# Kernel tuning notes

Measured on AMD Instinct MI355X. Metric: run time of the kernel, lower is better.

The kernel has to match this reference:

```python
import jax, jax.numpy as jnp
import numpy as np

NEG_INF = -1e30

def mask_logits(target, mask):
    return target * mask + (1.0 - mask) * NEG_INF

def setup_inputs() -> dict:
    key = jax.random.key(0)
    k1, k2, k3 = jax.random.split(key, 3)
    B, D, Lc, Lq = 32, 256, 2048, 256
    C = jax.random.normal(k1, (B, D, Lc), dtype=jnp.float32)
    Q = jax.random.normal(k2, (B, D, Lq), dtype=jnp.float32)
    cmask = jnp.ones((B, Lc), dtype=jnp.float32)
    qmask = jnp.ones((B, Lq), dtype=jnp.float32)
    lim = np.sqrt(1.0 / D)
    w = jax.random.uniform(k3, (3 * D,), dtype=jnp.float32, minval=-lim, maxval=lim)
    return {"C": C, "Q": Q, "cmask": cmask, "qmask": qmask, "w": w}

def reference(C, Q, cmask, qmask, w):
    # C: (B, D, Lc), Q: (B, D, Lq) -> transpose to (B, L, D)
    Ct = jnp.swapaxes(C, 1, 2)            # (B, Lc, D)
    Qt = jnp.swapaxes(Q, 1, 2)            # (B, Lq, D)
    D = Ct.shape[-1]
    w1, w2, w3 = w[:D], w[D:2 * D], w[2 * D:]
    # S[b,c,q] = Ct[b,c]@w1 + Qt[b,q]@w2 + (Ct[b,c]*w3)@Qt[b,q]
    # (identical to matmul(cat([Ct,Qt,Ct*Qt],-1), w) without the 4-D tensor)
    S = (Ct @ w1)[:, :, None] + (Qt @ w2)[:, None, :] \
        + jnp.einsum('bcd,bqd->bcq', Ct * w3, Qt)     # (B, Lc, Lq)
    qm = qmask[:, None, :]                 # (B, 1, Lq)
    cm = cmask[:, :, None]                 # (B, Lc, 1)
    S1 = jax.nn.softmax(mask_logits(S, qm), axis=2)   # over query dim
    S2 = jax.nn.softmax(mask_logits(S, cm), axis=1)   # over context dim
    A = jnp.einsum('bcq,bqd->bcd', S1, Qt)            # (B, Lc, D)
    Bv = jnp.einsum('bck,bkd->bcd',
                    jnp.einsum('bcq,bkq->bck', S1, S2), Ct)  # (B, Lc, D)
    out = jnp.concatenate([Ct, A, Ct * A, Ct * Bv], axis=2)  # (B, Lc, 4D)
    # dropout omitted (eval mode)
    return jnp.swapaxes(out, 1, 2)         # (B, 4D, Lc)
```

## Files before the change

### kernel.cpp

```cpp
#include <hip/hip_runtime.h>


#define B_ 32
#define D_ 256
#define LC 2048
#define LQ 256
#define KSPLIT 4
#define NEG_INF (-1e30f)

using bf16   = __bf16;
using bf16x4 = __attribute__((ext_vector_type(4))) __bf16;
using bf16x8 = __attribute__((ext_vector_type(8))) __bf16;
using f32x4  = __attribute__((ext_vector_type(4))) float;

static __device__ __forceinline__ f32x4 mfma16(bf16x8 a, bf16x8 b, f32x4 c) {
  return __builtin_amdgcn_mfma_f32_16x16x32_bf16(a, b, c, 0, 0, 0);
}

__global__ __launch_bounds__(256) void qprep(const float* __restrict__ Q,
                                             const float* __restrict__ w,
                                             bf16* __restrict__ Qtb,
                                             bf16* __restrict__ Qb16,
                                             float* __restrict__ bqp) {
  __shared__ float t[64][65];
  __shared__ float pb[4][64];
  const int b  = blockIdx.y;
  const int qt = (blockIdx.x >> 2) * 64;
  const int dtI = blockIdx.x & 3, dt = dtI * 64;
  const int c  = threadIdx.x & 63, r0 = threadIdx.x >> 6;
  const float* Qb = Q + (size_t)b * D_ * LQ;
  bf16* Qcb = Qb16 + (size_t)b * D_ * LQ;
  float partial = 0.f;
#pragma unroll
  for (int r = r0; r < 64; r += 4) {
    const float v = Qb[(size_t)(dt + r) * LQ + qt + c];
    t[r][c] = v;
    Qcb[(size_t)(dt + r) * LQ + qt + c] = (bf16)v;
    partial += v * w[D_ + dt + r];
  }
  pb[r0][c] = partial;
  __syncthreads();
  bf16* O = Qtb + (size_t)b * LQ * D_;
#pragma unroll
  for (int r = r0; r < 64; r += 4)
    O[(size_t)(qt + r) * D_ + dt + c] = (bf16)t[c][r];
  if (r0 == 0)
    bqp[((size_t)(b * 4 + dtI)) * LQ + qt + c] = pb[0][c] + pb[1][c] + pb[2][c] + pb[3][c];
}

__global__ __launch_bounds__(256) void k1_sgemm(
    const float* __restrict__ C, const bf16* __restrict__ Qtb,
    const float* __restrict__ w, const float* __restrict__ cmask,
    const float* __restrict__ qmask, const float* __restrict__ bqp,
    bf16* __restrict__ S1, bf16* __restrict__ S1t,
    float* __restrict__ cpmax, float* __restrict__ cpsum) {
  __shared__ __align__(16) bf16 As[64][72];
  __shared__ __align__(16) bf16 Bs[256][72];
  __shared__ float ared[4][64];
  __shared__ float wred[4][64];
  __shared__ float wsum[4][64];
  __shared__ float cml[64];
  __shared__ float qml[256];
  __shared__ float bql[256];

  const int b = blockIdx.y, ct = blockIdx.x, c0 = ct * 64;
  const int tid = threadIdx.x, lane = tid & 63, wv = tid >> 6;
  const float* Cb = C + (size_t)b * D_ * LC;
  const bf16* Qt = Qtb + (size_t)b * LQ * D_;
  const float* w1 = w;
  const float* w3 = w + 2 * D_;

  if (tid < 64) cml[tid] = cmask[b * LC + c0 + tid];
  qml[tid] = qmask[b * LQ + tid];
  bql[tid] = bqp[(size_t)(b * 4 + 0) * LQ + tid] + bqp[(size_t)(b * 4 + 1) * LQ + tid] +
             bqp[(size_t)(b * 4 + 2) * LQ + tid] + bqp[(size_t)(b * 4 + 3) * LQ + tid];

  f32x4 acc[4][4];
#pragma unroll
  for (int i = 0; i < 4; i++)
#pragma unroll
    for (int j = 0; j < 4; j++) acc[i][j] = {0.f, 0.f, 0.f, 0.f};
  float acc_a = 0.f;

  const int sm = tid & 63;
  const int skg = tid >> 6;

  for (int k0 = 0; k0 < D_; k0 += 64) {
#pragma unroll
    for (int i = 0; i < 16; ++i) {
      const int k = skg * 16 + i, kg = k0 + k;
      const float v = Cb[(size_t)kg * LC + c0 + sm];
      As[sm][k] = (bf16)(v * w3[kg]);
      acc_a += v * w1[kg];
    }
#pragma unroll
    for (int p = 0; p < 8; ++p) {
      const int idx = (p * 256 + tid) * 8;
      const int q = idx >> 6, kk = idx & 63;
      *(bf16x8*)(&Bs[q][kk]) = *(const bf16x8*)(Qt + (size_t)q * D_ + k0 + kk);
    }
    __syncthreads();
#pragma unroll
    for (int kk = 0; kk < 64; kk += 32) {
      bf16x8 af[4], bfr[4];
#pragma unroll
      for (int mi = 0; mi < 4; mi++)
        af[mi] = *(const bf16x8*)(&As[mi * 16 + (lane & 15)][kk + (lane >> 4) * 8]);
#pragma unroll
      for (int ni = 0; ni < 4; ni++)
        bfr[ni] = *(const bf16x8*)(&Bs[wv * 64 + ni * 16 + (lane & 15)][kk + (lane >> 4) * 8]);
#pragma unroll
      for (int mi = 0; mi < 4; mi++)
#pragma unroll
        for (int ni = 0; ni < 4; ni++)
          acc[mi][ni] = mfma16(af[mi], bfr[ni], acc[mi][ni]);
    }
    __syncthreads();
  }

  ared[skg][sm] = acc_a;
  __syncthreads();

  const int r4 = (lane >> 4) * 4;
  const int cn = lane & 15;

#pragma unroll
  for (int mi = 0; mi < 4; mi++)
#pragma unroll
    for (int j = 0; j < 4; j++) {
      const int m = mi * 16 + r4 + j;
      const float aval = ared[0][m] + ared[1][m] + ared[2][m] + ared[3][m];
#pragma unroll
      for (int ni = 0; ni < 4; ni++) {
        const int n = wv * 64 + ni * 16 + cn;
        const bf16 sb = (bf16)(acc[mi][ni][j] + aval + bql[n]);
        acc[mi][ni][j] = (float)sb;
      }
    }

#pragma unroll
  for (int ni = 0; ni < 4; ni++) {
    const int n = wv * 64 + ni * 16 + cn;
    float mx = -3.0e38f;
#pragma unroll
    for (int mi = 0; mi < 4; mi++)
#pragma unroll
      for (int j = 0; j < 4; j++) {
        const int m = mi * 16 + r4 + j;
        const float cmv = cml[m];
        const float lg = acc[mi][ni][j] * cmv + (1.f - cmv) * NEG_INF;
        mx = fmaxf(mx, lg);
      }
    mx = fmaxf(mx, __shfl_xor(mx, 16));
    mx = fmaxf(mx, __shfl_xor(mx, 32));
    float ps = 0.f;
#pragma unroll
    for (int mi = 0; mi < 4; mi++)
#pragma unroll
      for (int j = 0; j < 4; j++) {
        const int m = mi * 16 + r4 + j;
        const float cmv = cml[m];
        const float lg = acc[mi][ni][j] * cmv + (1.f - cmv) * NEG_INF;
        ps += __expf(lg - mx);
      }
    ps += __shfl_xor(ps, 16);
    ps += __shfl_xor(ps, 32);
    if ((lane >> 4) == 0) {
      cpmax[((size_t)(b * 32 + ct)) * LQ + n] = mx;
      cpsum[((size_t)(b * 32 + ct)) * LQ + n] = ps;
    }
  }

#pragma unroll
  for (int mi = 0; mi < 4; mi++)
#pragma unroll
    for (int j = 0; j < 4; j++) {
      float mx = -3.0e38f;
#pragma unroll
      for (int ni = 0; ni < 4; ni++) {
        const int n = wv * 64 + ni * 16 + cn;
        const float qm = qml[n];
        const float lg = acc[mi][ni][j] * qm + (1.f - qm) * NEG_INF;
        mx = fmaxf(mx, lg);
      }
      for (int s = 1; s < 16; s <<= 1) mx = fmaxf(mx, __shfl_xor(mx, s));
      if (cn == 0) wred[wv][mi * 16 + r4 + j] = mx;
    }
  __syncthreads();

  float rmv[4][4];
#pragma unroll
  for (int mi = 0; mi < 4; mi++)
#pragma unroll
    for (int j = 0; j < 4; j++) {
      const int m = mi * 16 + r4 + j;
      const float rm = fmaxf(fmaxf(wred[0][m], wred[1][m]), fmaxf(wred[2][m], wred[3][m]));
      rmv[mi][j] = rm;
      float ps = 0.f;
#pragma unroll
      for (int ni = 0; ni < 4; ni++) {
        const int n = wv * 64 + ni * 16 + cn;
        const float qm = qml[n];
        const float lg = acc[mi][ni][j] * qm + (1.f - qm) * NEG_INF;
        const float e = __expf(lg - rm);
        acc[mi][ni][j] = e;
        ps += e;
      }
      for (int s = 1; s < 16; s <<= 1) ps += __shfl_xor(ps, s);
      if (cn == 0) wsum[wv][m] = ps;
    }
  __syncthreads();

  bf16* S1b = S1 + ((size_t)b * LC + c0) * LQ;
#pragma unroll
  for (int mi = 0; mi < 4; mi++)
#pragma unroll
    for (int j = 0; j < 4; j++) {
      const int m = mi * 16 + r4 + j;
      const float rs = wsum[0][m] + wsum[1][m] + wsum[2][m] + wsum[3][m];
      const float rsl = 1.0f / rs;
      const float f = cml[m] * __expf(rmv[mi][j]);
#pragma unroll
      for (int ni = 0; ni < 4; ni++) {
        const int n = wv * 64 + ni * 16 + cn;
        const float e = acc[mi][ni][j];
        S1b[(size_t)m * LQ + n] = (bf16)(e * rsl);
        Bs[n][m] = (bf16)(e * f);
      }
    }
  __syncthreads();
  bf16* dst = S1t + ((size_t)b * LQ + tid) * LC + c0;
#pragma unroll
  for (int jj = 0; jj < 8; ++jj)
    *(bf16x8*)(dst + jj * 8) = *(const bf16x8*)(&Bs[tid][jj * 8]);
}

__global__ __launch_bounds__(256) void k2_colstats(const float* __restrict__ cpmax,
                                                   const float* __restrict__ cpsum,
                                                   float* __restrict__ cscl) {
  const int b = blockIdx.x, q = threadIdx.x;
  float m = -3.0e38f;
  for (int t = 0; t < 32; t++) m = fmaxf(m, cpmax[(size_t)(b * 32 + t) * LQ + q]);
  float s = 0.f;
  for (int t = 0; t < 32; t++)
    s += cpsum[(size_t)(b * 32 + t) * LQ + q] * __expf(cpmax[(size_t)(b * 32 + t) * LQ + q] - m);
  cscl[b * LQ + q] = __expf(-m) / s;
}

__global__ __launch_bounds__(256, 3) void k3_ugemm(
    const bf16* __restrict__ S1t, const float* __restrict__ C,
    float* __restrict__ Up) {
  const int g = blockIdx.x;
  const int x = g & 7, s = g >> 3;
  const int quad = (s >> 2) * 8 + x;
  const int inner = s & 3;
  const int b = quad >> 2, ks = quad & 3;
  const int qt = inner >> 1, dtI = inner & 1;
  const int mt = qt * 128, nt = dtI * 128;
  const int cbase = ks * (LC / KSPLIT);

  const int tid = threadIdx.x, lane = tid & 63, wv = tid >> 6;
  const int wm = (wv >> 1) * 64, wn = (wv & 1) * 64;
  const int fr = lane & 15, kg = lane >> 4;

  const bf16* Sb = S1t + (size_t)b * LQ * LC;
  const float* Cb = C + (size_t)b * D_ * LC;

  int qrow[4];
#pragma unroll
  for (int mi = 0; mi < 4; mi++) qrow[mi] = mt + wm + mi * 16 + fr;

  f32x4 acc[4][4];
#pragma unroll
  for (int i = 0; i < 4; i++)
#pragma unroll
    for (int j = 0; j < 4; j++) acc[i][j] = {0.f, 0.f, 0.f, 0.f};

#pragma unroll 2
  for (int k0 = 0; k0 < LC / KSPLIT; k0 += 64) {
    const int c8 = cbase + k0 + kg * 8;
    bf16x8 af[4][2];
#pragma unroll
    for (int mi = 0; mi < 4; mi++)
#pragma unroll
      for (int s2 = 0; s2 < 2; ++s2)
        af[mi][s2] = *(const bf16x8*)(Sb + (size_t)qrow[mi] * LC + c8 + s2 * 32);
    bf16x8 bfr[4][2];
#pragma unroll
    for (int ni = 0; ni < 4; ni++) {
      const float* cp = Cb + (size_t)(nt + wn + ni * 16 + fr) * LC + c8;
#pragma unroll
      for (int s2 = 0; s2 < 2; ++s2) {
        const f32x4 v0 = *(const f32x4*)(cp + s2 * 32);
        const f32x4 v1 = *(const f32x4*)(cp + s2 * 32 + 4);
        bf16x8 tt;
#pragma unroll
        for (int e = 0; e < 4; ++e) { tt[e] = (bf16)v0[e]; tt[e + 4] = (bf16)v1[e]; }
        bfr[ni][s2] = tt;
      }
    }
#pragma unroll
    for (int s2 = 0; s2 < 2; ++s2)
#pragma unroll
      for (int mi = 0; mi < 4; mi++)
#pragma unroll
        for (int ni = 0; ni < 4; ni++)
          acc[mi][ni] = mfma16(af[mi][s2], bfr[ni][s2], acc[mi][ni]);
  }

  float* Ub = Up + ((size_t)(ks * B_ + b)) * D_ * LQ;
#pragma unroll
  for (int mi = 0; mi < 4; mi++)
#pragma unroll
    for (int ni = 0; ni < 4; ni++) {
      const int q = mt + wm + mi * 16 + kg * 4;
      const int d = nt + wn + ni * 16 + fr;
      *(f32x4*)(Ub + (size_t)d * LQ + q) = acc[mi][ni];
    }
}

__global__ __launch_bounds__(256) void k3r_reduce(const float* __restrict__ Up,
                                                  const float* __restrict__ cscl,
                                                  bf16* __restrict__ Utb) {
  const size_t NP = (size_t)B_ * D_ * LQ;
  const size_t i4 = ((size_t)blockIdx.x * 256 + threadIdx.x) * 4;
  const int b = (int)(i4 >> 16);
  const int q = (int)(i4 & (LQ - 1));
  f32x4 s = *(const f32x4*)(Up + i4);
#pragma unroll
  for (int p = 1; p < KSPLIT; ++p) {
    const f32x4 v = *(const f32x4*)(Up + p * NP + i4);
    s[0] += v[0]; s[1] += v[1]; s[2] += v[2]; s[3] += v[3];
  }
  const f32x4 sc = *(const f32x4*)(cscl + b * LQ + q);
  bf16x4 o = {(bf16)(s[0] * sc[0]), (bf16)(s[1] * sc[1]),
              (bf16)(s[2] * sc[2]), (bf16)(s[3] * sc[3])};
  *(bf16x4*)(Utb + i4) = o;
}

__global__ __launch_bounds__(256, 3) void k4_final(
    const bf16* __restrict__ S1, const float* __restrict__ C,
    const bf16* __restrict__ Qb16, const bf16* __restrict__ Utb,
    float* __restrict__ out) {
  __shared__ float bounce[64][131];

  const int g = blockIdx.x;
  const int x = g & 7, s = g >> 3;
  const int t = s >> 1, ntI = s & 1;
  const int pair = t * 8 + x;
  const int b = pair >> 5, ct = pair & 31;
  const int c0 = ct * 64, nt = ntI * 128;

  const int tid = threadIdx.x, lane = tid & 63, wv = tid >> 6;
  const int wm = (wv >> 1) * 32, wn = (wv & 1) * 64;
  const int fr = lane & 15, kg = lane >> 4;

  const bf16* S1b = S1 + ((size_t)b * LC + c0) * LQ;
  const float* Cb = C + (size_t)b * D_ * LC;
  const bf16* Qcb = Qb16 + (size_t)b * D_ * LQ;
  const bf16* Ub = Utb + (size_t)b * D_ * LQ;

  f32x4 acc1[2][4], acc2[2][4];
#pragma unroll
  for (int i = 0; i < 2; i++)
#pragma unroll
    for (int j = 0; j < 4; j++) {
      acc1[i][j] = {0.f, 0.f, 0.f, 0.f};
      acc2[i][j] = {0.f, 0.f, 0.f, 0.f};
    }

#pragma unroll
  for (int k = 0; k < 8; ++k) {
    const int q8 = k * 32 + kg * 8;
    const bf16x8 af0 = *(const bf16x8*)(S1b + (size_t)(wm + fr) * LQ + q8);
    const bf16x8 af1 = *(const bf16x8*)(S1b + (size_t)(wm + 16 + fr) * LQ + q8);
#pragma unroll
    for (int ni = 0; ni < 4; ++ni) {
      const int d = nt + wn + ni * 16 + fr;
      const bf16x8 b1 = *(const bf16x8*)(Qcb + (size_t)d * LQ + q8);
      const bf16x8 b2 = *(const bf16x8*)(Ub + (size_t)d * LQ + q8);
      acc1[0][ni] = mfma16(af0, b1, acc1[0][ni]);
      acc1[1][ni] = mfma16(af1, b1, acc1[1][ni]);
      acc2[0][ni] = mfma16(af0, b2, acc2[0][ni]);
      acc2[1][ni] = mfma16(af1, b2, acc2[1][ni]);
    }
  }

  const int r4 = kg * 4;
#pragma unroll
  for (int mi = 0; mi < 2; mi++)
#pragma unroll
    for (int ni = 0; ni < 4; ni++)
#pragma unroll
      for (int j = 0; j < 4; j++)
        bounce[wm + mi * 16 + r4 + j][wn + ni * 16 + fr] = acc1[mi][ni][j];
  __syncthreads();

  const int cq = (tid & 15) * 4;
  const int drb = tid >> 4;
  const size_t outB = (size_t)b * (4 * D_) * LC;
  f32x4 creg[8];
#pragma unroll
  for (int m = 0; m < 8; ++m) {
    const int dr = drb + m * 16;
    const int d = nt + dr;
    f32x4 av;
#pragma unroll
    for (int e = 0; e < 4; ++e) av[e] = bounce[cq + e][dr];
    const f32x4 cv = *(const f32x4*)(Cb + (size_t)d * LC + c0 + cq);
    creg[m] = cv;
    f32x4 ca;
#pragma unroll
    for (int e = 0; e < 4; ++e) ca[e] = cv[e] * av[e];
    *(f32x4*)(out + outB + (size_t)d * LC + c0 + cq) = cv;
    *(f32x4*)(out + outB + (size_t)(D_ + d) * LC + c0 + cq) = av;
    *(f32x4*)(out + outB + (size_t)(2 * D_ + d) * LC + c0 + cq) = ca;
  }
  __syncthreads();
#pragma unroll
  for (int mi = 0; mi < 2; mi++)
#pragma unroll
    for (int ni = 0; ni < 4; ni++)
#pragma unroll
      for (int j = 0; j < 4; j++)
        bounce[wm + mi * 16 + r4 + j][wn + ni * 16 + fr] = acc2[mi][ni][j];
  __syncthreads();
#pragma unroll
  for (int m = 0; m < 8; ++m) {
    const int dr = drb + m * 16;
    const int d = nt + dr;
    f32x4 bv;
#pragma unroll
    for (int e = 0; e < 4; ++e) bv[e] = creg[m][e] * bounce[cq + e][dr];
    *(f32x4*)(out + outB + (size_t)(3 * D_ + d) * LC + c0 + cq) = bv;
  }
}

extern "C" void kernel_launch(void* const* d_in, const int* in_sizes, int n_in,
                              void* d_out, int out_size, void* d_ws, size_t ws_size,
                              hipStream_t stream) {
  (void)in_sizes; (void)n_in; (void)out_size; (void)ws_size;
  const float* C = (const float*)d_in[0];
  const float* Q = (const float*)d_in[1];
  const float* cmask = (const float*)d_in[2];
  const float* qmask = (const float*)d_in[3];
  const float* w = (const float*)d_in[4];
  float* out = (float*)d_out;

  float* ws = (float*)d_ws;
  float* Up = ws;
  float* cpm = Up + (size_t)KSPLIT * B_ * D_ * LQ;
  float* cps = cpm + B_ * 32 * LQ;
  float* cscl = cps + B_ * 32 * LQ;
  float* bqp = cscl + B_ * LQ;
  bf16* S1b = (bf16*)(bqp + B_ * 4 * LQ);
  bf16* S1tb = S1b + (size_t)B_ * LC * LQ;
  bf16* Utb = S1tb + (size_t)B_ * LC * LQ;
  bf16* Qb16 = Utb + (size_t)B_ * D_ * LQ;
  bf16* Qtb = (bf16*)Up;

  qprep<<<dim3(16, B_), 256, 0, stream>>>(Q, w, Qtb, Qb16, bqp);
  k1_sgemm<<<dim3(LC / 64, B_), 256, 0, stream>>>(C, Qtb, w, cmask, qmask, bqp,
                                                  S1b, S1tb, cpm, cps);
  k2_colstats<<<dim3(B_), 256, 0, stream>>>(cpm, cps, cscl);
  k3_ugemm<<<dim3(16 * B_), 256, 0, stream>>>(S1tb, C, Up);
  k3r_reduce<<<dim3((B_ * D_ * LQ) / 1024), 256, 0, stream>>>(Up, cscl, Utb);
  k4_final<<<dim3(64 * B_), 256, 0, stream>>>(S1b, C, Qb16, Utb, out);
}
```

Before: 250.9 us.

## Double-buffer C tile in k1 and load Q fragments directly from global

The S-GEMM kernel now double-buffers the scaled C tile in shared memory, prefetching the next K-slice while MFMAs run on the current one. This leaves one barrier per iteration instead of two. Q fragments are read straight from global/L2 into registers rather than staged through a shared tile. The freed LDS is unioned with the transpose bounce buffer, which shrinks the shared footprint and may raise occupancy. In exchange, Q reads become uncoalesced 16-byte gathers from global memory, and register pressure rises from holding two K-steps of fragments.

```diff
diff --git a/kernel.cpp b/kernel.cpp
--- a/kernel.cpp
+++ b/kernel.cpp
@@ -54,8 +54,10 @@
     const float* __restrict__ qmask, const float* __restrict__ bqp,
     bf16* __restrict__ S1, bf16* __restrict__ S1t,
     float* __restrict__ cpmax, float* __restrict__ cpsum) {
-  __shared__ __align__(16) bf16 As[64][72];
-  __shared__ __align__(16) bf16 Bs[256][72];
+  __shared__ union __align__(16) SmU {
+    bf16 As[2][64][72];
+    bf16 Bounce[256][72];
+  } smu;
   __shared__ float ared[4][64];
   __shared__ float wred[4][64];
   __shared__ float wsum[4][64];
@@ -84,45 +86,58 @@
 
   const int sm = tid & 63;
   const int skg = tid >> 6;
-
-  for (int k0 = 0; k0 < D_; k0 += 64) {
-#pragma unroll
-    for (int i = 0; i < 16; ++i) {
-      const int k = skg * 16 + i, kg = k0 + k;
-      const float v = Cb[(size_t)kg * LC + c0 + sm];
-      As[sm][k] = (bf16)(v * w3[kg]);
-      acc_a += v * w1[kg];
-    }
-#pragma unroll
-    for (int p = 0; p < 8; ++p) {
-      const int idx = (p * 256 + tid) * 8;
-      const int q = idx >> 6, kk = idx & 63;
-      *(bf16x8*)(&Bs[q][kk]) = *(const bf16x8*)(Qt + (size_t)q * D_ + k0 + kk);
-    }
+  const int fr = lane & 15, kg = lane >> 4;
+
+#pragma unroll
+  for (int i = 0; i < 16; ++i) {
+    const int k = skg * 16 + i;
+    const float v = Cb[(size_t)k * LC + c0 + sm];
+    smu.As[0][sm][k] = (bf16)(v * w3[k]);
+    acc_a += v * w1[k];
+  }
+  __syncthreads();
+
+  int bufI = 0;
+#pragma unroll
+  for (int it = 0; it < 4; ++it) {
+    const int k0 = it * 64;
+    if (it < 3) {
+#pragma unroll
+      for (int i = 0; i < 16; ++i) {
+        const int k = skg * 16 + i, kg2 = k0 + 64 + k;
+        const float v = Cb[(size_t)kg2 * LC + c0 + sm];
+        smu.As[bufI ^ 1][sm][k] = (bf16)(v * w3[kg2]);
+        acc_a += v * w1[kg2];
+      }
+    }
+    bf16x8 bfr[2][4], af[2][4];
+#pragma unroll
+    for (int ks = 0; ks < 2; ++ks)
+#pragma unroll
+      for (int ni = 0; ni < 4; ++ni)
+        bfr[ks][ni] = *(const bf16x8*)(Qt + (size_t)(wv * 64 + ni * 16 + fr) * D_ +
+                                       k0 + ks * 32 + kg * 8);
+#pragma unroll
+    for (int ks = 0; ks < 2; ++ks)
+#pragma unroll
+      for (int mi = 0; mi < 4; ++mi)
+        af[ks][mi] = *(const bf16x8*)(&smu.As[bufI][mi * 16 + fr][ks * 32 + kg * 8]);
+#pragma unroll
+    for (int ks = 0; ks < 2; ++ks)
+#pragma unroll
+      for (int mi = 0; mi < 4; mi++)
+#pragma unroll
+        for (int ni = 0; ni < 4; ni++)
+          acc[mi][ni] = mfma16(af[ks][mi], bfr[ks][ni], acc[mi][ni]);
     __syncthreads();
-#pragma unroll
-    for (int kk = 0; kk < 64; kk += 32) {
-      bf16x8 af[4], bfr[4];
-#pragma unroll
-      for (int mi = 0; mi < 4; mi++)
-        af[mi] = *(const bf16x8*)(&As[mi * 16 + (lane & 15)][kk + (lane >> 4) * 8]);
-#pragma unroll
-      for (int ni = 0; ni < 4; ni++)
-        bfr[ni] = *(const bf16x8*)(&Bs[wv * 64 + ni * 16 + (lane & 15)][kk + (lane >> 4) * 8]);
-#pragma unroll
-      for (int mi = 0; mi < 4; mi++)
-#pragma unroll
-        for (int ni = 0; ni < 4; ni++)
-          acc[mi][ni] = mfma16(af[mi], bfr[ni], acc[mi][ni]);
-    }
-    __syncthreads();
+    bufI ^= 1;
   }
 
   ared[skg][sm] = acc_a;
   __syncthreads();
 
-  const int r4 = (lane >> 4) * 4;
-  const int cn = lane & 15;
+  const int r4 = kg * 4;
+  const int cn = fr;
 
 #pragma unroll
   for (int mi = 0; mi < 4; mi++)
@@ -165,7 +180,7 @@
       }
     ps += __shfl_xor(ps, 16);
     ps += __shfl_xor(ps, 32);
-    if ((lane >> 4) == 0) {
+    if (kg == 0) {
       cpmax[((size_t)(b * 32 + ct)) * LQ + n] = mx;
       cpsum[((size_t)(b * 32 + ct)) * LQ + n] = ps;
     }
@@ -225,14 +240,14 @@
         const int n = wv * 64 + ni * 16 + cn;
         const float e = acc[mi][ni][j];
         S1b[(size_t)m * LQ + n] = (bf16)(e * rsl);
-        Bs[n][m] = (bf16)(e * f);
+        smu.Bounce[n][m] = (bf16)(e * f);
       }
     }
   __syncthreads();
   bf16* dst = S1t + ((size_t)b * LQ + tid) * LC + c0;
 #pragma unroll
   for (int jj = 0; jj < 8; ++jj)
-    *(bf16x8*)(dst + jj * 8) = *(const bf16x8*)(&Bs[tid][jj * 8]);
+    *(bf16x8*)(dst + jj * 8) = *(const bf16x8*)(&smu.Bounce[tid][jj * 8]);
 }
 
 __global__ __launch_bounds__(256) void k2_colstats(const float* __restrict__ cpmax,
```

After: 282.7 us. 12.7% more time.

## Prefetch next K-tile into registers in score kernel and hoist C loads in output kernel

Applied to the files above, without the earlier changes.

The score kernel's K loop now loads the next 64-wide slice of C and Qt into registers right after the barrier, so those global loads overlap the MFMA work on the current tile instead of stalling at the start of each iteration. The output kernel issues its C loads before the MFMA loop, so their latency is hidden behind the matmul rather than paid in the epilogue. Both changes add roughly 48 registers per thread for the prefetch buffers plus 32 for creg, which can lower occupancy or cause spills.

```diff
diff --git a/kernel.cpp b/kernel.cpp
--- a/kernel.cpp
+++ b/kernel.cpp
@@ -85,21 +85,41 @@
   const int sm = tid & 63;
   const int skg = tid >> 6;
 
-  for (int k0 = 0; k0 < D_; k0 += 64) {
+  float aPre[16];
+  bf16x8 bPre[8];
+#pragma unroll
+  for (int i = 0; i < 16; ++i)
+    aPre[i] = Cb[(size_t)(skg * 16 + i) * LC + c0 + sm];
+#pragma unroll
+  for (int p = 0; p < 8; ++p) {
+    const int idx = (p * 256 + tid) * 8;
+    bPre[p] = *(const bf16x8*)(Qt + (size_t)(idx >> 6) * D_ + (idx & 63));
+  }
+
+  for (int it = 0; it < 4; ++it) {
+    const int k0 = it * 64;
 #pragma unroll
     for (int i = 0; i < 16; ++i) {
-      const int k = skg * 16 + i, kg = k0 + k;
-      const float v = Cb[(size_t)kg * LC + c0 + sm];
-      As[sm][k] = (bf16)(v * w3[kg]);
-      acc_a += v * w1[kg];
+      const int k = skg * 16 + i, kgl = k0 + k;
+      As[sm][k] = (bf16)(aPre[i] * w3[kgl]);
+      acc_a += aPre[i] * w1[kgl];
     }
 #pragma unroll
     for (int p = 0; p < 8; ++p) {
       const int idx = (p * 256 + tid) * 8;
-      const int q = idx >> 6, kk = idx & 63;
-      *(bf16x8*)(&Bs[q][kk]) = *(const bf16x8*)(Qt + (size_t)q * D_ + k0 + kk);
+      *(bf16x8*)(&Bs[idx >> 6][idx & 63]) = bPre[p];
     }
     __syncthreads();
+    if (it < 3) {
+#pragma unroll
+      for (int i = 0; i < 16; ++i)
+        aPre[i] = Cb[(size_t)(k0 + 64 + skg * 16 + i) * LC + c0 + sm];
+#pragma unroll
+      for (int p = 0; p < 8; ++p) {
+        const int idx = (p * 256 + tid) * 8;
+        bPre[p] = *(const bf16x8*)(Qt + (size_t)(idx >> 6) * D_ + k0 + 64 + (idx & 63));
+      }
+    }
 #pragma unroll
     for (int kk = 0; kk < 64; kk += 32) {
       bf16x8 af[4], bfr[4];
@@ -360,6 +380,13 @@
   const bf16* Qcb = Qb16 + (size_t)b * D_ * LQ;
   const bf16* Ub = Utb + (size_t)b * D_ * LQ;
 
+  const int cq = (tid & 15) * 4;
+  const int drb = tid >> 4;
+  f32x4 creg[8];
+#pragma unroll
+  for (int m = 0; m < 8; ++m)
+    creg[m] = *(const f32x4*)(Cb + (size_t)(nt + drb + m * 16) * LC + c0 + cq);
+
   f32x4 acc1[2][4], acc2[2][4];
 #pragma unroll
   for (int i = 0; i < 2; i++)
@@ -396,10 +423,7 @@
         bounce[wm + mi * 16 + r4 + j][wn + ni * 16 + fr] = acc1[mi][ni][j];
   __syncthreads();
 
-  const int cq = (tid & 15) * 4;
-  const int drb = tid >> 4;
   const size_t outB = (size_t)b * (4 * D_) * LC;
-  f32x4 creg[8];
 #pragma unroll
   for (int m = 0; m < 8; ++m) {
     const int dr = drb + m * 16;
@@ -407,8 +431,7 @@
     f32x4 av;
 #pragma unroll
     for (int e = 0; e < 4; ++e) av[e] = bounce[cq + e][dr];
-    const f32x4 cv = *(const f32x4*)(Cb + (size_t)d * LC + c0 + cq);
-    creg[m] = cv;
+    const f32x4 cv = creg[m];
     f32x4 ca;
 #pragma unroll
     for (int e = 0; e < 4; ++e) ca[e] = cv[e] * av[e];
```

Measured after the change: 246.7 us. No clear change (-1.6%).
